# Kernel tuning notes

Hardware: AMD Instinct MI355X
Metric: run time of the kernel (lower is better)

Reference implementation:

```python
import jax, jax.numpy as jnp
import numpy as np

B, NO, NM = 16, 512, 32
DO, DM, DOUT = 128, 64, 128   # in_ope_dim, in_mac_dim, out_mac_dim
H, K = 64, 16                  # external attn: num_heads*coef=8*8, k=dim//num_heads
HID = 128                      # policy hidden dim
NEG = jnp.float32(-1e30)


def _lin(x, W, b=None):
    y = x @ W.T
    return y + b if b is not None else y


def external_attention(x, W_trans, b_trans, W_l0, b_l0, W_l1, b_l1, W_proj, b_proj):
    Bx, N, C = x.shape
    x = _lin(x, W_trans, b_trans)                      # [B,N,8C]
    x = x.reshape(Bx, N, H, K).transpose(0, 2, 1, 3)   # [B,H,N,K]
    attn = _lin(x, W_l0, b_l0)
    attn = jax.nn.softmax(attn, axis=-2)               # softmax over N
    attn = attn / (1e-10 + attn.sum(-1, keepdims=True))
    x = _lin(attn, W_l1, b_l1).transpose(0, 2, 1, 3).reshape(Bx, N, H * K)
    return _lin(x, W_proj, b_proj)                     # [B,N,C]


def gat(adj, feat_ope, feat_mac, Wo, Wm, alpha_o, alpha_m):
    h_ope = feat_ope @ Wo.T                            # [B,No,D]
    h_mac = feat_mac @ Wm.T                            # [B,Nm,D]
    a_o = (h_ope * alpha_o).sum(-1)                    # [B,No]
    a_m = (h_mac * alpha_m).sum(-1)                    # [B,Nm]
    e = adj * (a_o[:, :, None] + a_m[:, None, :])      # [B,No,Nm]
    e = jnp.where(e >= 0, e, 0.2 * e)                  # leaky_relu(0.2)
    mask = adj == 1.0
    e = jnp.where(mask, e, jnp.float32(-9e10))
    alpha = jax.nn.softmax(e, axis=-2) * mask          # softmax over opes
    out_ope = jnp.einsum('bom,bod->bmd', alpha, h_ope) # [B,Nm,D]
    return out_ope + h_mac


def mlp(x, Ws, bs):
    for W, b in zip(Ws[:-1], bs[:-1]):
        x = jnp.tanh(x @ W.T + b)
    return x @ Ws[-1].T + bs[-1]


def setup_inputs() -> dict:
    key = jax.random.key(0)
    ks = jax.random.split(key, 24)
    d = {}
    d['curr_proc_adj'] = jax.random.randint(ks[0], (B, NO, NM), 0, 2).astype(jnp.float32)
    d['norm_opes'] = jax.random.normal(ks[1], (B, NO, DO), jnp.float32)
    d['norm_macs'] = jax.random.normal(ks[2], (B, NM, DM), jnp.float32)
    mask_proc = jax.random.randint(ks[3], (B, NO, NM), 0, 2).astype(bool)
    d['mask_proc'] = mask_proc
    # choose valid (unmasked) actions in the flattened [Nm, No] layout
    mask_flat = jnp.swapaxes(mask_proc, 1, 2).reshape(B, -1)
    d['action_indexes'] = jnp.argmax(mask_flat, axis=1).astype(jnp.int32)
    s = 0.05
    # external attention params (torch Linear: [out,in])
    d['W_trans'] = s * jax.random.normal(ks[4], (DO * 8, DO)); d['b_trans'] = jnp.zeros((DO * 8,))
    d['W_l0'] = s * jax.random.normal(ks[5], (K, K)); d['b_l0'] = jnp.zeros((K,))
    d['W_l1'] = s * jax.random.normal(ks[6], (K, K)); d['b_l1'] = jnp.zeros((K,))
    d['W_proj'] = s * jax.random.normal(ks[7], (DO, DO * 8)); d['b_proj'] = jnp.zeros((DO,))
    # GAT params
    d['Wo'] = s * jax.random.normal(ks[8], (DOUT, DO))
    d['Wm'] = s * jax.random.normal(ks[9], (DOUT, DM))
    d['alpha_o'] = s * jax.random.normal(ks[10], (1, 1, DOUT))
    d['alpha_m'] = s * jax.random.normal(ks[11], (1, 1, DOUT))
    # actor MLP: 512 -> 128 -> 128 -> 1
    d['A0'] = s * jax.random.normal(ks[12], (HID, 2 * DO + 2 * DOUT)); d['Ab0'] = jnp.zeros((HID,))
    d['A1'] = s * jax.random.normal(ks[13], (HID, HID)); d['Ab1'] = jnp.zeros((HID,))
    d['A2'] = s * jax.random.normal(ks[14], (1, HID)); d['Ab2'] = jnp.zeros((1,))
    # critic MLP: 256 -> 128 -> 128 -> 1
    d['C0'] = s * jax.random.normal(ks[15], (HID, DO + DOUT)); d['Cb0'] = jnp.zeros((HID,))
    d['C1'] = s * jax.random.normal(ks[16], (HID, HID)); d['Cb1'] = jnp.zeros((HID,))
    d['C2'] = s * jax.random.normal(ks[17], (1, HID)); d['Cb2'] = jnp.zeros((1,))
    return d


def reference(curr_proc_adj, norm_opes, norm_macs, mask_proc, action_indexes,
              W_trans, b_trans, W_l0, b_l0, W_l1, b_l1, W_proj, b_proj,
              Wo, Wm, alpha_o, alpha_m,
              A0, Ab0, A1, Ab1, A2, Ab2, C0, Cb0, C1, Cb1, C2, Cb2):
    h_opes = external_attention(norm_opes, W_trans, b_trans, W_l0, b_l0,
                                W_l1, b_l1, W_proj, b_proj)      # [B,No,DO]
    h_macs = gat(curr_proc_adj, norm_opes, norm_macs, Wo, Wm, alpha_o, alpha_m)  # [B,Nm,DOUT]
    h_opes_pooled = h_opes.mean(-2)   # [B,DO]
    h_macs_pooled = h_macs.mean(-2)   # [B,DOUT]
    # build h_actions directly in transposed [B, Nm, No, :] layout
    sh_o = (B, NM, NO, DO); sh_m = (B, NM, NO, DOUT)
    h_actions = jnp.concatenate([
        jnp.broadcast_to(h_opes[:, None, :, :], sh_o),
        jnp.broadcast_to(h_macs[:, :, None, :], sh_m),
        jnp.broadcast_to(h_opes_pooled[:, None, None, :], sh_o),
        jnp.broadcast_to(h_macs_pooled[:, None, None, :], sh_m)], axis=-1)
    logits = mlp(h_actions, [A0, A1, A2], [Ab0, Ab1, Ab2]).reshape(B, -1)  # [B, Nm*No]
    mask = jnp.swapaxes(mask_proc, 1, 2).reshape(B, -1)
    logits = jnp.where(mask, logits, NEG)
    logp = jax.nn.log_softmax(logits, axis=1)
    p = jnp.exp(logp)
    action_logprobs = jnp.take_along_axis(logp, action_indexes[:, None], axis=1)[:, 0]
    dist_entropys = -jnp.sum(jnp.where(mask, p * logp, 0.0), axis=1)
    h_pooled = jnp.concatenate([h_opes_pooled, h_macs_pooled], axis=-1)  # [B,256]
    state_values = mlp(h_pooled, [C0, C1, C2], [Cb0, Cb1, Cb2])[:, 0]
    return action_logprobs, state_values, dist_entropys
```

## Files before the change

### kernel.cpp

```cpp
#include <hip/hip_runtime.h>

#define BB 16
#define NO 512
#define NM 32
#define DOC 128
#define C8 1024
#define NH 64
#define KD 16

#define OFF_X12   0
#define OFF_UO    0
#define OFF_LOG   1048576
#define OFF_HOPES 8388608
#define OFF_HOPEG 9437184
#define OFF_HMAC  10485760
#define OFF_HMACS 10551296
#define OFF_AO    10616832
#define OFF_AM    10625024
#define OFF_PO    10625536
#define OFF_PM    10627584
#define OFF_UMHM  10629632
#define OFF_FLAG  10695168
#define OFF_UP    10720000
#define OFF_PART2 10750000
#define OFF_A1P   10900000

using f32x4  = __attribute__((ext_vector_type(4))) float;
using s16x4  = __attribute__((ext_vector_type(4))) short;
using bf16x8 = __attribute__((ext_vector_type(8))) short;

__device__ __forceinline__ float fast_tanh(float x) {
  float e = __expf(2.0f * x);
  return 1.0f - 2.0f * __builtin_amdgcn_rcpf(e + 1.0f);
}

__device__ __forceinline__ short f2bf(float f) {
  unsigned u = __builtin_bit_cast(unsigned, f);
  u += 0x7FFFu + ((u >> 16) & 1u);
  return (short)(u >> 16);
}

__device__ __forceinline__ float bf2f(short s) {
  return __builtin_bit_cast(float, ((unsigned)(unsigned short)s) << 16);
}

__device__ __forceinline__ unsigned cvtpk(float a, float b) {
  unsigned r;
  asm("v_cvt_pk_bf16_f32 %0, %1, %2" : "=v"(r) : "v"(a), "v"(b));
  return r;
}

__device__ __forceinline__ bf16x8 pack8(f32x4 u0, f32x4 u1) {
  union { unsigned u[4]; bf16x8 v; } cv;
  cv.u[0] = cvtpk(u0[0], u0[1]);
  cv.u[1] = cvtpk(u0[2], u0[3]);
  cv.u[2] = cvtpk(u1[0], u1[1]);
  cv.u[3] = cvtpk(u1[2], u1[3]);
  return cv.v;
}

__device__ __forceinline__ bf16x8 pack8f(const float* t) {
  union { unsigned u[4]; bf16x8 v; } cv;
  cv.u[0] = cvtpk(t[0], t[1]);
  cv.u[1] = cvtpk(t[2], t[3]);
  cv.u[2] = cvtpk(t[4], t[5]);
  cv.u[3] = cvtpk(t[6], t[7]);
  return cv.v;
}

__device__ __forceinline__ void smmerge(float& lm, float& lS, float& lT,
                                        float om, float oS, float oT) {
  float nm = fmaxf(lm, om);
  float ea = __expf(lm - nm), eb = __expf(om - nm);
  lT = (lT + (lm - nm) * lS) * ea + (oT + (om - nm) * oS) * eb;
  lS = lS * ea + oS * eb;
  lm = nm;
}

__device__ void probe_body(int tid, const unsigned int* __restrict__ mask,
                           int* __restrict__ flag) {
  __shared__ int s[4];
  int bad = 0;
  for (int i = tid; i < 4096; i += 256) {
    unsigned int v = mask[i];
    if (!(v == 0u || v == 1u || v == 0x3f800000u)) bad = 1;
  }
  unsigned long long any = __ballot(bad);
  int lane = tid & 63, w = tid >> 6;
  if (lane == 0) s[w] = (any != 0ull) ? 1 : 0;
  __syncthreads();
  if (tid == 0) flag[0] = s[0] | s[1] | s[2] | s[3];
}

template<int MT>
__device__ __forceinline__ void loadk(const float* xb, const float* wb,
                                      long sx, long sw, int k0,
                                      f32x4 (&xa)[MT][2], f32x4 (&wa)[4][2]) {
  #pragma unroll
  for (int mi = 0; mi < MT; ++mi) {
    xa[mi][0] = *(const f32x4*)(xb + mi * sx + k0);
    xa[mi][1] = *(const f32x4*)(xb + mi * sx + k0 + 4);
  }
  #pragma unroll
  for (int ni = 0; ni < 4; ++ni) {
    wa[ni][0] = *(const f32x4*)(wb + ni * sw + k0);
    wa[ni][1] = *(const f32x4*)(wb + ni * sw + k0 + 4);
  }
}

template<int MT>
__device__ __forceinline__ void consume(f32x4 (&xa)[MT][2], f32x4 (&wa)[4][2],
                                        f32x4 (&acc)[MT][4]) {
  bf16x8 bfr[4];
  #pragma unroll
  for (int ni = 0; ni < 4; ++ni) bfr[ni] = pack8(wa[ni][0], wa[ni][1]);
  #pragma unroll
  for (int mi = 0; mi < MT; ++mi) {
    bf16x8 af = pack8(xa[mi][0], xa[mi][1]);
    #pragma unroll
    for (int ni = 0; ni < 4; ++ni)
      acc[mi][ni] = __builtin_amdgcn_mfma_f32_16x16x32_bf16(af, bfr[ni], acc[mi][ni], 0, 0, 0);
  }
}

template<int MT>
__device__ void gemm_wave_body(int bx, int by, int tid,
    const float* __restrict__ X, const float* __restrict__ W,
    const float* __restrict__ bias, float* __restrict__ C,
    int N, int Kdim, int ldx, int ldw) {
  const int lane = tid & 63, w = tid >> 6;
  const int rowl = lane & 15, kg = lane >> 4;
  const int n0 = bx * 64;
  const int m0 = (by * 4 + w) * (MT * 16);
  const float* xb = X + (long)(m0 + rowl) * ldx + kg * 8;
  const float* wb = W + (long)(n0 + rowl) * ldw + kg * 8;
  const long sx = (long)16 * ldx, sw = (long)16 * ldw;
  f32x4 acc[MT][4] = {};
  f32x4 A0[MT][2], B0[4][2], A1[MT][2], B1[4][2];
  loadk<MT>(xb, wb, sx, sw, 0, A0, B0);
  for (int k = 0; k < Kdim; k += 64) {
    loadk<MT>(xb, wb, sx, sw, k + 32, A1, B1);
    consume<MT>(A0, B0, acc);
    if (k + 64 < Kdim) loadk<MT>(xb, wb, sx, sw, k + 64, A0, B0);
    consume<MT>(A1, B1, acc);
  }
  #pragma unroll
  for (int mi = 0; mi < MT; ++mi) {
    #pragma unroll
    for (int ni = 0; ni < 4; ++ni) {
      int col = n0 + ni * 16 + rowl;
      float bv = bias ? bias[col] : 0.0f;
      int rb = m0 + mi * 16 + kg * 4;
      #pragma unroll
      for (int r = 0; r < 4; ++r)
        C[(long)(rb + r) * N + col] = acc[mi][ni][r] + bv;
    }
  }
}

template<int MT>
__device__ void gemm_ht_body(int bx, int by, int tid,
    const float* __restrict__ X, const float* __restrict__ W,
    const float* __restrict__ bias, short* __restrict__ Ch,
    int Kdim, int ldx, int ldw) {
  const int lane = tid & 63, w = tid >> 6;
  const int rowl = lane & 15, kg = lane >> 4;
  const int n0 = bx * 64;
  const int m0 = (by * 4 + w) * (MT * 16);
  const float* xb = X + (long)(m0 + rowl) * ldx + kg * 8;
  const float* wb = W + (long)(n0 + rowl) * ldw + kg * 8;
  const long sx = (long)16 * ldx, sw = (long)16 * ldw;
  f32x4 acc[MT][4] = {};
  f32x4 A0[MT][2], B0[4][2], A1[MT][2], B1[4][2];
  loadk<MT>(xb, wb, sx, sw, 0, A0, B0);
  for (int k = 0; k < Kdim; k += 64) {
    loadk<MT>(xb, wb, sx, sw, k + 32, A1, B1);
    consume<MT>(A0, B0, acc);
    if (k + 64 < Kdim) loadk<MT>(xb, wb, sx, sw, k + 64, A0, B0);
    consume<MT>(A1, B1, acc);
  }
  #pragma unroll
  for (int mi = 0; mi < MT; ++mi) {
    #pragma unroll
    for (int ni = 0; ni < 4; ++ni) {
      int col = n0 + ni * 16 + rowl;
      float bv = bias ? bias[col] : 0.0f;
      int h = col >> 4, e = col & 15;
      int rb = m0 + mi * 16 + kg * 4;
      #pragma unroll
      for (int r = 0; r < 4; ++r) {
        int rowI = rb + r;
        int b = rowI >> 9, n = rowI & 511;
        Ch[((long)(b * 64 + h) * 512 + n) * 16 + e] = f2bf(acc[mi][ni][r] + bv);
      }
    }
  }
}

__device__ void convert_a1_body(int blk, int tid,
    const float* __restrict__ A1, short* __restrict__ A1p) {
  int i = blk * 256 + tid;
  int col = i >> 7, k = i & 127;
  A1p[((k >> 3) * 128 + col) * 8 + (k & 7)] = f2bf(A1[i]);
}

__global__ __launch_bounds__(256) void mega1_kernel(
    const float* __restrict__ nop, const float* __restrict__ Wtr,
    const float* __restrict__ btr, short* __restrict__ x12h,
    const float* __restrict__ Wo, float* __restrict__ hopeG,
    const float* __restrict__ nmac, const float* __restrict__ Wm,
    float* __restrict__ hmac,
    const float* __restrict__ A1, short* __restrict__ A1p,
    const unsigned int* __restrict__ mask, int* __restrict__ flag) {
  const int blk = blockIdx.x, tid = threadIdx.x;
  if (blk < 512) {
    gemm_ht_body<4>(blk & 15, blk >> 4, tid, nop, Wtr, btr, x12h, 128, 128, 128);
  } else if (blk < 768) {
    int t = blk - 512;
    gemm_wave_body<1>(t & 1, t >> 1, tid, nop, Wo, nullptr, hopeG, 128, 128, 128, 128);
  } else if (blk < 784) {
    int t = blk - 768;
    gemm_wave_body<1>(t & 1, t >> 1, tid, nmac, Wm, nullptr, hmac, 128, 64, 64, 64);
  } else if (blk < 848) {
    convert_a1_body(blk - 784, tid, A1, A1p);
  } else {
    probe_body(tid, mask, flag);
  }
}

__device__ void attn3_body(int b, int h, int tid, short* __restrict__ x12h,
    const float* __restrict__ W0, const float* __restrict__ b0,
    const float* __restrict__ W1, const float* __restrict__ b1) {
  __shared__ short Pb[4][128 * 16];
  __shared__ float cmw[4][16], csw[4][16];
  const int wq = tid >> 6, lane = tid & 63;
  const int rowl = lane & 15, kg = lane >> 4;
  short* slice = x12h + (long)(b * 64 + h) * 8192;
  const short* wrows = slice + (long)(wq * 128) * 16;
  const bf16x8 zero8 = {};
  bf16x8 xa[8];
  #pragma unroll
  for (int t = 0; t < 8; ++t) {
    if (kg < 2)
      xa[t] = *(const bf16x8*)(wrows + (t * 16 + rowl) * 16 + kg * 8);
    else
      xa[t] = zero8;
  }
  bf16x8 w0f = zero8;
  if (kg < 2) {
    f32x4 a = *(const f32x4*)(W0 + rowl * 16 + kg * 8);
    f32x4 c = *(const f32x4*)(W0 + rowl * 16 + kg * 8 + 4);
    w0f = pack8(a, c);
  }
  const float b0v = b0[rowl];
  f32x4 acc[8];
  #pragma unroll
  for (int t = 0; t < 8; ++t) {
    f32x4 z = {0.f, 0.f, 0.f, 0.f};
    acc[t] = __builtin_amdgcn_mfma_f32_16x16x32_bf16(xa[t], w0f, z, 0, 0, 0);
  }
  float m = -1e30f;
  #pragma unroll
  for (int t = 0; t < 8; ++t)
    #pragma unroll
    for (int r = 0; r < 4; ++r) {
      acc[t][r] += b0v;
      m = fmaxf(m, acc[t][r]);
    }
  m = fmaxf(m, __shfl_xor(m, 16));
  m = fmaxf(m, __shfl_xor(m, 32));
  if (lane < 16) cmw[wq][lane] = m;
  __syncthreads();
  const float cm = fmaxf(fmaxf(cmw[0][rowl], cmw[1][rowl]),
                         fmaxf(cmw[2][rowl], cmw[3][rowl]));
  float s = 0.f;
  #pragma unroll
  for (int t = 0; t < 8; ++t)
    #pragma unroll
    for (int r = 0; r < 4; ++r) {
      float e = __expf(acc[t][r] - cm);
      acc[t][r] = e;
      s += e;
    }
  s += __shfl_xor(s, 16);
  s += __shfl_xor(s, 32);
  if (lane < 16) csw[wq][lane] = s;
  __syncthreads();
  const float cs = csw[0][rowl] + csw[1][rowl] + csw[2][rowl] + csw[3][rowl];
  const float cinv = 1.0f / cs;
  short* pbw = Pb[wq];
  #pragma unroll
  for (int t = 0; t < 8; ++t)
    #pragma unroll
    for (int r = 0; r < 4; ++r) {
      float al = acc[t][r] * cinv;
      float rsv = al;
      rsv += __shfl_xor(rsv, 1);
      rsv += __shfl_xor(rsv, 2);
      rsv += __shfl_xor(rsv, 4);
      rsv += __shfl_xor(rsv, 8);
      float pf = al / (1e-10f + rsv);
      pbw[(t * 16 + kg * 4 + r) * 16 + rowl] = f2bf(pf);
    }
  __syncthreads();
  bf16x8 w1f = zero8;
  if (kg < 2) {
    f32x4 a = *(const f32x4*)(W1 + rowl * 16 + kg * 8);
    f32x4 c = *(const f32x4*)(W1 + rowl * 16 + kg * 8 + 4);
    w1f = pack8(a, c);
  }
  const float b1v = b1[rowl];
  #pragma unroll
  for (int t = 0; t < 8; ++t) {
    bf16x8 pa = zero8;
    if (kg < 2)
      pa = *(const bf16x8*)(pbw + (t * 16 + rowl) * 16 + kg * 8);
    f32x4 z = {0.f, 0.f, 0.f, 0.f};
    f32x4 oacc = __builtin_amdgcn_mfma_f32_16x16x32_bf16(pa, w1f, z, 0, 0, 0);
    #pragma unroll
    for (int r = 0; r < 4; ++r) {
      int n = wq * 128 + t * 16 + kg * 4 + r;
      slice[(long)n * 16 + rowl] = f2bf(oacc[r] + b1v);
    }
  }
}

__global__ __launch_bounds__(256) void mega2_kernel(
    short* __restrict__ x12h,
    const float* __restrict__ W0, const float* __restrict__ b0,
    const float* __restrict__ W1, const float* __restrict__ b1,
    const float* __restrict__ hopeG, const float* __restrict__ alo,
    float* __restrict__ ao,
    const float* __restrict__ hmac, const float* __restrict__ alm,
    float* __restrict__ am) {
  const int blk = blockIdx.x, tid = threadIdx.x;
  if (blk < 1024) {
    attn3_body(blk >> 6, blk & 63, tid, x12h, W0, b0, W1, b1);
  } else {
    int t = blk - 1024;
    int wid = t * 4 + (tid >> 6);
    int lane = tid & 63;
    const float* X; const float* al; float* out; int r;
    if (wid < 8192)       { X = hopeG; al = alo; out = ao; r = wid; }
    else if (wid < 8704)  { X = hmac;  al = alm; out = am; r = wid - 8192; }
    else return;
    const float* row = X + (long)r * 128;
    float v = fmaf(row[lane], al[lane], row[lane + 64] * al[lane + 64]);
    #pragma unroll
    for (int off = 32; off; off >>= 1) v += __shfl_down(v, off);
    if (lane == 0) out[r] = v;
  }
}

__device__ void gemm_hx_body(int bx, int by, int tid,
    const short* __restrict__ Xh, const float* __restrict__ W,
    const float* __restrict__ bias, float* __restrict__ C) {
  const int lane = tid & 63, w = tid >> 6;
  const int rowl = lane & 15, kg = lane >> 4;
  const int n0 = bx * 64;
  const int m0 = (by * 4 + w) * 16;
  const int row = m0 + rowl, b = row >> 9, n = row & 511;
  const short* xb = Xh + (long)b * 524288 + (long)n * 16 + (kg & 1) * 8;
  const long hofs = kg >> 1;
  const float* wb = W + (long)(n0 + rowl) * 1024 + kg * 8;
  const long sw = 16 * 1024L;
  f32x4 acc[4] = {};
  bf16x8 A0, A1;
  f32x4 Wb0[4][2], Wb1[4][2];
  A0 = *(const bf16x8*)(xb + hofs * 8192);
  #pragma unroll
  for (int ni = 0; ni < 4; ++ni) {
    Wb0[ni][0] = *(const f32x4*)(wb + ni * sw);
    Wb0[ni][1] = *(const f32x4*)(wb + ni * sw + 4);
  }
  for (int k = 0; k < 1024; k += 64) {
    A1 = *(const bf16x8*)(xb + (((k + 32) >> 4) + hofs) * 8192);
    #pragma unroll
    for (int ni = 0; ni < 4; ++ni) {
      Wb1[ni][0] = *(const f32x4*)(wb + ni * sw + k + 32);
      Wb1[ni][1] = *(const f32x4*)(wb + ni * sw + k + 36);
    }
    #pragma unroll
    for (int ni = 0; ni < 4; ++ni) {
      bf16x8 bfr = pack8(Wb0[ni][0], Wb0[ni][1]);
      acc[ni] = __builtin_amdgcn_mfma_f32_16x16x32_bf16(A0, bfr, acc[ni], 0, 0, 0);
    }
    if (k + 64 < 1024) {
      A0 = *(const bf16x8*)(xb + (((k + 64) >> 4) + hofs) * 8192);
      #pragma unroll
      for (int ni = 0; ni < 4; ++ni) {
        Wb0[ni][0] = *(const f32x4*)(wb + ni * sw + k + 64);
        Wb0[ni][1] = *(const f32x4*)(wb + ni * sw + k + 68);
      }
    }
    #pragma unroll
    for (int ni = 0; ni < 4; ++ni) {
      bf16x8 bfr = pack8(Wb1[ni][0], Wb1[ni][1]);
      acc[ni] = __builtin_amdgcn_mfma_f32_16x16x32_bf16(A1, bfr, acc[ni], 0, 0, 0);
    }
  }
  #pragma unroll
  for (int ni = 0; ni < 4; ++ni) {
    int col = n0 + ni * 16 + rowl;
    float bv = bias ? bias[col] : 0.0f;
    int rb = m0 + kg * 4;
    #pragma unroll
    for (int r = 0; r < 4; ++r)
      C[(long)(rb + r) * 128 + col] = acc[ni][r] + bv;
  }
}

__device__ void gat_body(int b, int m, int tid,
    const float* __restrict__ adj, const float* __restrict__ ao,
    const float* __restrict__ am, const float* __restrict__ hopeG,
    const float* __restrict__ hmac, float* __restrict__ hmacs) {
  __shared__ float al[NO];
  __shared__ float redA[4], redB[4];
  __shared__ float part[2][128];
  const int lane = tid & 63, w = tid >> 6;
  const float amv = am[b * NM + m];
  float av[2], ev[2];
  float mx = -1e30f;
  #pragma unroll
  for (int i = 0; i < 2; ++i) {
    int o = tid + i * 256;
    float a = adj[(b * NO + o) * NM + m];
    float e = ao[b * NO + o] + amv;
    e = (e >= 0.f) ? e : 0.2f * e;
    av[i] = a; ev[i] = e;
    if (a == 1.0f) mx = fmaxf(mx, e);
  }
  #pragma unroll
  for (int off = 32; off; off >>= 1) mx = fmaxf(mx, __shfl_down(mx, off));
  if (lane == 0) redA[w] = mx;
  __syncthreads();
  mx = fmaxf(fmaxf(redA[0], redA[1]), fmaxf(redA[2], redA[3]));
  float p[2], s = 0.f;
  #pragma unroll
  for (int i = 0; i < 2; ++i) {
    p[i] = (av[i] == 1.0f) ? __expf(ev[i] - mx) : 0.f;
    s += p[i];
  }
  #pragma unroll
  for (int off = 32; off; off >>= 1) s += __shfl_down(s, off);
  if (lane == 0) redB[w] = s;
  __syncthreads();
  s = redB[0] + redB[1] + redB[2] + redB[3];
  const float sinv = (s > 0.f) ? 1.0f / s : 0.f;
  al[tid] = p[0] * sinv;
  al[tid + 256] = p[1] * sinv;
  __syncthreads();
  const int d = tid & 127, og = tid >> 7;
  float acc0 = 0.f, acc1 = 0.f;
  const float* hb = hopeG + ((long)(b * NO) + og * 256) * DOC + d;
  #pragma unroll 8
  for (int i = 0; i < 256; i += 2) {
    acc0 = fmaf(al[og * 256 + i],     hb[(long)i * DOC],       acc0);
    acc1 = fmaf(al[og * 256 + i + 1], hb[(long)(i + 1) * DOC], acc1);
  }
  part[og][d] = acc0 + acc1;
  __syncthreads();
  if (og == 0)
    hmacs[(b * NM + m) * DOC + d] = part[0][d] + part[1][d]
                                   + hmac[(b * NM + m) * DOC + d];
}

__global__ __launch_bounds__(256) void mega3_kernel(
    const short* __restrict__ x12h, const float* __restrict__ Wp,
    const float* __restrict__ bp, float* __restrict__ hopes,
    const float* __restrict__ adj, const float* __restrict__ ao,
    const float* __restrict__ am, const float* __restrict__ hopeG,
    const float* __restrict__ hmac, float* __restrict__ hmacs) {
  const int blk = blockIdx.x, tid = threadIdx.x;
  if (blk < 256) {
    gemm_hx_body(blk & 1, blk >> 1, tid, x12h, Wp, bp, hopes);
  } else {
    int t = blk - 256;
    gat_body(t & 15, t >> 4, tid,
             adj, ao, am, hopeG, hmac, hmacs);
  }
}

__device__ void pool_up_body(int b, int tid,
    const float* __restrict__ hopes, const float* __restrict__ hmacs,
    const float* __restrict__ A0, const float* __restrict__ Ab0,
    float* __restrict__ po, float* __restrict__ pm, float* __restrict__ up) {
  __shared__ float part[2][128];
  __shared__ float pos[128], pms[128];
  const int j = tid & 127, og = tid >> 7;
  const float* hb = hopes + ((long)(b * 512) + og * 256) * 128 + j;
  float a0 = 0.f, a1 = 0.f;
  #pragma unroll 8
  for (int i = 0; i < 256; i += 2) {
    a0 += hb[(long)i * 128];
    a1 += hb[(long)(i + 1) * 128];
  }
  part[og][j] = a0 + a1;
  __syncthreads();
  if (og == 0) {
    float s = (part[0][j] + part[1][j]) * (1.0f / 512.0f);
    po[b * 128 + j] = s;
    pos[j] = s;
  } else {
    const float* mb = hmacs + (long)(b * 32) * 128 + j;
    float t0 = 0.f;
    #pragma unroll 8
    for (int i = 0; i < 32; ++i) t0 += mb[(long)i * 128];
    t0 *= (1.0f / 32.0f);
    pm[b * 128 + j] = t0;
    pms[j] = t0;
  }
  __syncthreads();
  if (tid < 128) {
    const float* a1p = A0 + (long)j * 512 + 256;
    const float* a2p = A0 + (long)j * 512 + 384;
    float acc = Ab0[j];
    #pragma unroll 4
    for (int k4 = 0; k4 < 32; ++k4) {
      f32x4 av = *(const f32x4*)(a1p + k4 * 4);
      acc = fmaf(av[0], pos[k4 * 4], acc);
      acc = fmaf(av[1], pos[k4 * 4 + 1], acc);
      acc = fmaf(av[2], pos[k4 * 4 + 2], acc);
      acc = fmaf(av[3], pos[k4 * 4 + 3], acc);
    }
    #pragma unroll 4
    for (int k4 = 0; k4 < 32; ++k4) {
      f32x4 av = *(const f32x4*)(a2p + k4 * 4);
      acc = fmaf(av[0], pms[k4 * 4], acc);
      acc = fmaf(av[1], pms[k4 * 4 + 1], acc);
      acc = fmaf(av[2], pms[k4 * 4 + 2], acc);
      acc = fmaf(av[3], pms[k4 * 4 + 3], acc);
    }
    up[b * 128 + j] = acc;
  }
}

__global__ __launch_bounds__(256) void mega4_kernel(
    const float* __restrict__ hopes, const float* __restrict__ hmacs,
    const float* __restrict__ A0, const float* __restrict__ Ab0,
    float* __restrict__ po, float* __restrict__ pm, float* __restrict__ up,
    float* __restrict__ Uo, float* __restrict__ umhm) {
  const int blk = blockIdx.x, tid = threadIdx.x;
  if (blk < 16) {
    pool_up_body(blk, tid, hopes, hmacs, A0, Ab0, po, pm, up);
  } else if (blk < 272) {
    int t = blk - 16;
    gemm_wave_body<1>(t & 1, t >> 1, tid, hopes, A0, nullptr, Uo, 128, 128, 128, 512);
  } else {
    int t = blk - 272;
    gemm_wave_body<1>(t & 1, t >> 1, tid, hmacs, A0 + 128, nullptr, umhm, 128, 128, 128, 512);
  }
}

__global__ __launch_bounds__(256) void actor_mfma9_kernel(
    const float* __restrict__ Uo, const float* __restrict__ umhm,
    const float* __restrict__ up, const short* __restrict__ A1p,
    const float* __restrict__ Ab1, const float* __restrict__ A2,
    const float* __restrict__ Ab2, const void* __restrict__ maskp,
    const int* __restrict__ flag, float* __restrict__ logits,
    float* __restrict__ partw) {
  const int tid = threadIdx.x;
  const int blk = blockIdx.x;
  const int oc = blk & 7;
  const int mg = (blk >> 3) & 7;
  const int b  = blk >> 6;
  const int obase = oc * 64;
  const int m0 = mg * 4;
  const int lane = tid & 63, w = tid >> 6;
  const int rowl = lane & 15, kg = lane >> 4;
  const float* uo = Uo + (long)(b * NO + obase + w * 16 + rowl) * 128;
  const float* upb = up + b * 128;
  const float* umb = umhm + (b * NM + m0) * 128;
  bf16x8 af[4][4];
  #pragma unroll
  for (int kk = 0; kk < 4; ++kk) {
    int kb = kk * 32 + kg * 8;
    f32x4 u0 = *(const f32x4*)(uo + kb);
    f32x4 u1 = *(const f32x4*)(uo + kb + 4);
    f32x4 p0 = *(const f32x4*)(upb + kb);
    f32x4 p1 = *(const f32x4*)(upb + kb + 4);
    float base0[4], base1[4];
    #pragma unroll
    for (int e = 0; e < 4; ++e) {
      base0[e] = u0[e] + p0[e];
      base1[e] = u1[e] + p1[e];
    }
    #pragma unroll
    for (int mi = 0; mi < 4; ++mi) {
      f32x4 a0 = *(const f32x4*)(umb + mi * 128 + kb);
      f32x4 a1 = *(const f32x4*)(umb + mi * 128 + kb + 4);
      float t[8];
      #pragma unroll
      for (int e = 0; e < 4; ++e) {
        t[e]     = fast_tanh(base0[e] + a0[e]);
        t[4 + e] = fast_tanh(base1[e] + a1[e]);
      }
      af[mi][kk] = pack8f(t);
    }
  }
  float pr[4][4] = {};
  #pragma unroll
  for (int ct = 0; ct < 8; ++ct) {
    const int col = ct * 16 + rowl;
    bf16x8 bf[4];
    #pragma unroll
    for (int kk = 0; kk < 4; ++kk)
      bf[kk] = *(const bf16x8*)(A1p + ((kk * 4 + kg) * 128 + col) * 8);
    f32x4 ac[4] = {};
    #pragma unroll
    for (int kk = 0; kk < 4; ++kk)
      #pragma unroll
      for (int mi = 0; mi < 4; ++mi)
        ac[mi] = __builtin_amdgcn_mfma_f32_16x16x32_bf16(af[mi][kk], bf[kk], ac[mi], 0, 0, 0);
    const float ab = Ab1[col], a2c = A2[col];
    #pragma unroll
    for (int mi = 0; mi < 4; ++mi)
      #pragma unroll
      for (int r = 0; r < 4; ++r) {
        float z = fast_tanh(ac[mi][r] + ab);
        pr[mi][r] = fmaf(a2c, z, pr[mi][r]);
      }
  }
  const float ab2 = Ab2[0];
  float rv[4][4];
  #pragma unroll
  for (int r = 0; r < 4; ++r) {
    float v0 = pr[0][r], v1 = pr[1][r], v2 = pr[2][r], v3 = pr[3][r];
    #pragma unroll
    for (int off = 1; off < 16; off <<= 1) {
      v0 += __shfl_xor(v0, off);
      v1 += __shfl_xor(v1, off);
      v2 += __shfl_xor(v2, off);
      v3 += __shfl_xor(v3, off);
    }
    rv[r][0] = v0 + ab2; rv[r][1] = v1 + ab2;
    rv[r][2] = v2 + ab2; rv[r][3] = v3 + ab2;
  }
  const long base0 = ((long)b << 14) + (long)m0 * 512 + obase + w * 16 + kg * 4;
  if (rowl == 0) {
    #pragma unroll
    for (int r = 0; r < 4; ++r) {
      logits[base0 + r]        = rv[r][0];
      logits[base0 + 512 + r]  = rv[r][1];
      logits[base0 + 1024 + r] = rv[r][2];
      logits[base0 + 1536 + r] = rv[r][3];
    }
  }
  const bool word_mode = (flag[0] == 0);
  const int ob = obase + w * 16 + kg * 4;
  bool mk[4][4];
  if (word_mode) {
    const unsigned int* mw = (const unsigned int*)maskp;
    #pragma unroll
    for (int r = 0; r < 4; ++r) {
      long mo = (long)(b * NO + ob + r) * NM + m0;
      #pragma unroll
      for (int mi = 0; mi < 4; ++mi) mk[r][mi] = (mw[mo + mi] != 0u);
    }
  } else {
    const unsigned char* mb = (const unsigned char*)maskp;
    #pragma unroll
    for (int r = 0; r < 4; ++r) {
      long mo = (long)(b * NO + ob + r) * NM + m0;
      #pragma unroll
      for (int mi = 0; mi < 4; ++mi) mk[r][mi] = (mb[mo + mi] != 0);
    }
  }
  float lm = -1e30f;
  #pragma unroll
  for (int r = 0; r < 4; ++r)
    #pragma unroll
    for (int mi = 0; mi < 4; ++mi)
      if (mk[r][mi]) lm = fmaxf(lm, rv[r][mi]);
  float lS = 0.f, lT = 0.f;
  #pragma unroll
  for (int r = 0; r < 4; ++r)
    #pragma unroll
    for (int mi = 0; mi < 4; ++mi)
      if (mk[r][mi]) {
        float d = rv[r][mi] - lm;
        float e = __expf(d);
        lS += e; lT += e * d;
      }
  #pragma unroll
  for (int off = 16; off < 64; off <<= 1) {
    float om = __shfl_xor(lm, off);
    float oS = __shfl_xor(lS, off);
    float oT = __shfl_xor(lT, off);
    smmerge(lm, lS, lT, om, oS, oT);
  }
  if (lane == 0) {
    float* pp = partw + ((long)blk * 4 + w) * 3;
    pp[0] = lm; pp[1] = lS; pp[2] = lT;
  }
}

__global__ __launch_bounds__(128) void final2c_kernel(
    const float* __restrict__ part, const float* __restrict__ logits,
    const int* __restrict__ aidx,
    const float* __restrict__ po, const float* __restrict__ pm,
    const float* __restrict__ C0, const float* __restrict__ Cb0,
    const float* __restrict__ C1, const float* __restrict__ Cb1,
    const float* __restrict__ C2, const float* __restrict__ Cb2,
    float* __restrict__ out) {
  if (blockIdx.x < 16) {
    if (threadIdx.x >= 64) return;
    const int b = blockIdx.x;
    const int lane = threadIdx.x;
    float lm = -3e30f, lS = 0.f, lT = 0.f;
    const float* pp = part + ((long)b * 256 + lane * 4) * 3;
    #pragma unroll
    for (int t = 0; t < 4; ++t)
      smmerge(lm, lS, lT, pp[t * 3], pp[t * 3 + 1], pp[t * 3 + 2]);
    #pragma unroll
    for (int off = 1; off < 64; off <<= 1) {
      float om = __shfl_xor(lm, off);
      float oS = __shfl_xor(lS, off);
      float oT = __shfl_xor(lT, off);
      smmerge(lm, lS, lT, om, oS, oT);
    }
    if (lane == 0) {
      float lSm = logf(lS);
      out[b] = logits[b * (NM * NO) + aidx[b]] - lm - lSm;
      out[32 + b] = lSm - lT / lS;
    }
  } else {
    __shared__ float v[256];
    __shared__ float z[128];
    __shared__ float sc[2];
    const int b = blockIdx.x - 16;
    const int j = threadIdx.x;
    v[j] = po[b * 128 + j];
    v[128 + j] = pm[b * 128 + j];
    __syncthreads();
    float acc = Cb0[j];
    for (int k = 0; k < 256; ++k) acc = fmaf(C0[j * 256 + k], v[k], acc);
    z[j] = fast_tanh(acc);
    __syncthreads();
    acc = Cb1[j];
    for (int k = 0; k < 128; ++k) acc = fmaf(C1[j * 128 + k], z[k], acc);
    float z2 = fast_tanh(acc);
    float p = C2[j] * z2;
    #pragma unroll
    for (int off = 32; off; off >>= 1) p += __shfl_down(p, off);
    const int lane = j & 63, w = j >> 6;
    if (lane == 0) sc[w] = p;
    __syncthreads();
    if (j == 0) out[16 + b] = sc[0] + sc[1] + Cb2[0];
  }
}

extern "C" void kernel_launch(void* const* d_in, const int* in_sizes, int n_in,
                              void* d_out, int out_size, void* d_ws, size_t ws_size,
                              hipStream_t stream) {
  (void)in_sizes; (void)n_in; (void)out_size; (void)ws_size;
  const float* adj  = (const float*)d_in[0];
  const float* nop  = (const float*)d_in[1];
  const float* nmac = (const float*)d_in[2];
  const void*  maskp = d_in[3];
  const int*   aidx = (const int*)d_in[4];
  const float* Wtr  = (const float*)d_in[5];
  const float* btr  = (const float*)d_in[6];
  const float* W0   = (const float*)d_in[7];
  const float* b0   = (const float*)d_in[8];
  const float* W1   = (const float*)d_in[9];
  const float* b1   = (const float*)d_in[10];
  const float* Wp   = (const float*)d_in[11];
  const float* bp   = (const float*)d_in[12];
  const float* Wo   = (const float*)d_in[13];
  const float* Wm   = (const float*)d_in[14];
  const float* alo  = (const float*)d_in[15];
  const float* alm  = (const float*)d_in[16];
  const float* A0   = (const float*)d_in[17];
  const float* Ab0  = (const float*)d_in[18];
  const float* A1   = (const float*)d_in[19];
  const float* Ab1  = (const float*)d_in[20];
  const float* A2   = (const float*)d_in[21];
  const float* Ab2  = (const float*)d_in[22];
  const float* C0   = (const float*)d_in[23];
  const float* Cb0  = (const float*)d_in[24];
  const float* C1   = (const float*)d_in[25];
  const float* Cb1  = (const float*)d_in[26];
  const float* C2   = (const float*)d_in[27];
  const float* Cb2  = (const float*)d_in[28];

  float* ws     = (float*)d_ws;
  short* x12h   = (short*)(ws + OFF_X12);
  float* hopes  = ws + OFF_HOPES;
  float* hopeG  = ws + OFF_HOPEG;
  float* hmac   = ws + OFF_HMAC;
  float* hmacs  = ws + OFF_HMACS;
  float* ao     = ws + OFF_AO;
  float* am     = ws + OFF_AM;
  float* po     = ws + OFF_PO;
  float* pm     = ws + OFF_PM;
  float* Uo     = ws + OFF_UO;
  float* umhm   = ws + OFF_UMHM;
  float* logits = ws + OFF_LOG;
  float* up     = ws + OFF_UP;
  short* A1p    = (short*)(ws + OFF_A1P);
  int*   flag   = (int*)(ws + OFF_FLAG);
  float* partw  = ws + OFF_PART2;
  float* outp   = (float*)d_out;

  mega1_kernel<<<849, 256, 0, stream>>>(nop, Wtr, btr, x12h, Wo, hopeG,
                                        nmac, Wm, hmac, A1, A1p,
                                        (const unsigned int*)maskp, flag);
  mega2_kernel<<<3200, 256, 0, stream>>>(x12h, W0, b0, W1, b1,
                                         hopeG, alo, ao, hmac, alm, am);
  mega3_kernel<<<768, 256, 0, stream>>>(x12h, Wp, bp, hopes,
                                        adj, ao, am, hopeG, hmac, hmacs);
  mega4_kernel<<<288, 256, 0, stream>>>(hopes, hmacs, A0, Ab0,
                                        po, pm, up, Uo, umhm);
  actor_mfma9_kernel<<<1024, 256, 0, stream>>>(Uo, umhm, up, A1p, Ab1, A2, Ab2,
                                               maskp, flag, logits, partw);
  final2c_kernel<<<32, 128, 0, stream>>>(partw, logits, aidx,
                                         po, pm, C0, Cb0, C1, Cb1, C2, Cb2, outp);
}
```

Before: 138.7 us.

## Remove final kernel by fusing critic MLP and last-block logsumexp reduction

Moves the critic MLP into the pooling blocks of mega4, which already hold the pooled vectors in shared memory. The per-batch log-softmax combine now runs inside the actor kernel: an atomic counter, zeroed in mega1, lets the last of the 64 blocks per batch merge the partials and write the outputs. This removes one kernel launch and its dependency gap. In exchange it adds threadfence/atomic overhead to every actor block and makes the 16 pooling blocks longer, which may delay mega4 slightly.

```diff
diff --git a/kernel.cpp b/kernel.cpp
--- a/kernel.cpp
+++ b/kernel.cpp
@@ -21,6 +21,7 @@
 #define OFF_PM    10627584
 #define OFF_UMHM  10629632
 #define OFF_FLAG  10695168
+#define OFF_CNT   10695680
 #define OFF_UP    10720000
 #define OFF_PART2 10750000
 #define OFF_A1P   10900000
@@ -78,8 +79,9 @@
 }
 
 __device__ void probe_body(int tid, const unsigned int* __restrict__ mask,
-                           int* __restrict__ flag) {
+                           int* __restrict__ flag, int* __restrict__ cnt) {
   __shared__ int s[4];
+  if (tid < 16) cnt[tid] = 0;
   int bad = 0;
   for (int i = tid; i < 4096; i += 256) {
     unsigned int v = mask[i];
@@ -211,7 +213,8 @@
     const float* __restrict__ nmac, const float* __restrict__ Wm,
     float* __restrict__ hmac,
     const float* __restrict__ A1, short* __restrict__ A1p,
-    const unsigned int* __restrict__ mask, int* __restrict__ flag) {
+    const unsigned int* __restrict__ mask, int* __restrict__ flag,
+    int* __restrict__ cnt) {
   const int blk = blockIdx.x, tid = threadIdx.x;
   if (blk < 512) {
     gemm_ht_body<4>(blk & 15, blk >> 4, tid, nop, Wtr, btr, x12h, 128, 128, 128);
@@ -224,7 +227,7 @@
   } else if (blk < 848) {
     convert_a1_body(blk - 784, tid, A1, A1p);
   } else {
-    probe_body(tid, mask, flag);
+    probe_body(tid, mask, flag, cnt);
   }
 }
 
@@ -484,9 +487,15 @@
 __device__ void pool_up_body(int b, int tid,
     const float* __restrict__ hopes, const float* __restrict__ hmacs,
     const float* __restrict__ A0, const float* __restrict__ Ab0,
-    float* __restrict__ po, float* __restrict__ pm, float* __restrict__ up) {
+    const float* __restrict__ C0, const float* __restrict__ Cb0,
+    const float* __restrict__ C1, const float* __restrict__ Cb1,
+    const float* __restrict__ C2, const float* __restrict__ Cb2,
+    float* __restrict__ po, float* __restrict__ pm, float* __restrict__ up,
+    float* __restrict__ out) {
   __shared__ float part[2][128];
   __shared__ float pos[128], pms[128];
+  __shared__ float zc[128];
+  __shared__ float scc[2];
   const int j = tid & 127, og = tid >> 7;
   const float* hb = hopes + ((long)(b * 512) + og * 256) * 128 + j;
   float a0 = 0.f, a1 = 0.f;
@@ -532,17 +541,39 @@
       acc = fmaf(av[3], pms[k4 * 4 + 3], acc);
     }
     up[b * 128 + j] = acc;
-  }
+    float cacc = Cb0[j];
+    for (int k = 0; k < 128; ++k) cacc = fmaf(C0[j * 256 + k], pos[k], cacc);
+    for (int k = 0; k < 128; ++k) cacc = fmaf(C0[j * 256 + 128 + k], pms[k], cacc);
+    zc[j] = fast_tanh(cacc);
+  }
+  __syncthreads();
+  if (tid < 128) {
+    float acc2 = Cb1[j];
+    for (int k = 0; k < 128; ++k) acc2 = fmaf(C1[j * 128 + k], zc[k], acc2);
+    float z2 = fast_tanh(acc2);
+    float p = C2[j] * z2;
+    #pragma unroll
+    for (int off = 32; off; off >>= 1) p += __shfl_down(p, off);
+    const int lane = tid & 63, w = tid >> 6;
+    if (lane == 0) scc[w] = p;
+  }
+  __syncthreads();
+  if (tid == 0) out[16 + b] = scc[0] + scc[1] + Cb2[0];
 }
 
 __global__ __launch_bounds__(256) void mega4_kernel(
     const float* __restrict__ hopes, const float* __restrict__ hmacs,
     const float* __restrict__ A0, const float* __restrict__ Ab0,
+    const float* __restrict__ C0, const float* __restrict__ Cb0,
+    const float* __restrict__ C1, const float* __restrict__ Cb1,
+    const float* __restrict__ C2, const float* __restrict__ Cb2,
     float* __restrict__ po, float* __restrict__ pm, float* __restrict__ up,
-    float* __restrict__ Uo, float* __restrict__ umhm) {
+    float* __restrict__ Uo, float* __restrict__ umhm,
+    float* __restrict__ out) {
   const int blk = blockIdx.x, tid = threadIdx.x;
   if (blk < 16) {
-    pool_up_body(blk, tid, hopes, hmacs, A0, Ab0, po, pm, up);
+    pool_up_body(blk, tid, hopes, hmacs, A0, Ab0, C0, Cb0, C1, Cb1, C2, Cb2,
+                 po, pm, up, out);
   } else if (blk < 272) {
     int t = blk - 16;
     gemm_wave_body<1>(t & 1, t >> 1, tid, hopes, A0, nullptr, Uo, 128, 128, 128, 512);
@@ -552,13 +583,14 @@
   }
 }
 
-__global__ __launch_bounds__(256) void actor_mfma9_kernel(
+__global__ __launch_bounds__(256) void actor_mfma10_kernel(
     const float* __restrict__ Uo, const float* __restrict__ umhm,
     const float* __restrict__ up, const short* __restrict__ A1p,
     const float* __restrict__ Ab1, const float* __restrict__ A2,
     const float* __restrict__ Ab2, const void* __restrict__ maskp,
-    const int* __restrict__ flag, float* __restrict__ logits,
-    float* __restrict__ partw) {
+    const int* __restrict__ flag, const int* __restrict__ aidx,
+    float* __restrict__ logits, float* __restrict__ partw,
+    int* __restrict__ cnt, float* __restrict__ out) {
   const int tid = threadIdx.x;
   const int blk = blockIdx.x;
   const int oc = blk & 7;
@@ -693,60 +725,33 @@
     float* pp = partw + ((long)blk * 4 + w) * 3;
     pp[0] = lm; pp[1] = lS; pp[2] = lT;
   }
-}
-
-__global__ __launch_bounds__(128) void final2c_kernel(
-    const float* __restrict__ part, const float* __restrict__ logits,
-    const int* __restrict__ aidx,
-    const float* __restrict__ po, const float* __restrict__ pm,
-    const float* __restrict__ C0, const float* __restrict__ Cb0,
-    const float* __restrict__ C1, const float* __restrict__ Cb1,
-    const float* __restrict__ C2, const float* __restrict__ Cb2,
-    float* __restrict__ out) {
-  if (blockIdx.x < 16) {
-    if (threadIdx.x >= 64) return;
-    const int b = blockIdx.x;
-    const int lane = threadIdx.x;
-    float lm = -3e30f, lS = 0.f, lT = 0.f;
-    const float* pp = part + ((long)b * 256 + lane * 4) * 3;
+  __shared__ int sdone;
+  __syncthreads();
+  if (tid == 0) {
+    __threadfence();
+    int old = atomicAdd((int*)&cnt[b], 1);
+    sdone = (old == 63) ? 1 : 0;
+  }
+  __syncthreads();
+  if (sdone && tid < 64) {
+    __threadfence();
+    float fm = -3e30f, fS = 0.f, fT = 0.f;
+    const float* pp = partw + ((long)b * 256 + tid * 4) * 3;
     #pragma unroll
     for (int t = 0; t < 4; ++t)
-      smmerge(lm, lS, lT, pp[t * 3], pp[t * 3 + 1], pp[t * 3 + 2]);
+      smmerge(fm, fS, fT, pp[t * 3], pp[t * 3 + 1], pp[t * 3 + 2]);
     #pragma unroll
     for (int off = 1; off < 64; off <<= 1) {
-      float om = __shfl_xor(lm, off);
-      float oS = __shfl_xor(lS, off);
-      float oT = __shfl_xor(lT, off);
-      smmerge(lm, lS, lT, om, oS, oT);
-    }
-    if (lane == 0) {
-      float lSm = logf(lS);
-      out[b] = logits[b * (NM * NO) + aidx[b]] - lm - lSm;
-      out[32 + b] = lSm - lT / lS;
-    }
-  } else {
-    __shared__ float v[256];
-    __shared__ float z[128];
-    __shared__ float sc[2];
-    const int b = blockIdx.x - 16;
-    const int j = threadIdx.x;
-    v[j] = po[b * 128 + j];
-    v[128 + j] = pm[b * 128 + j];
-    __syncthreads();
-    float acc = Cb0[j];
-    for (int k = 0; k < 256; ++k) acc = fmaf(C0[j * 256 + k], v[k], acc);
-    z[j] = fast_tanh(acc);
-    __syncthreads();
-    acc = Cb1[j];
-    for (int k = 0; k < 128; ++k) acc = fmaf(C1[j * 128 + k], z[k], acc);
-    float z2 = fast_tanh(acc);
-    float p = C2[j] * z2;
-    #pragma unroll
-    for (int off = 32; off; off >>= 1) p += __shfl_down(p, off);
-    const int lane = j & 63, w = j >> 6;
-    if (lane == 0) sc[w] = p;
-    __syncthreads();
-    if (j == 0) out[16 + b] = sc[0] + sc[1] + Cb2[0];
+      float om = __shfl_xor(fm, off);
+      float oS = __shfl_xor(fS, off);
+      float oT = __shfl_xor(fT, off);
+      smmerge(fm, fS, fT, om, oS, oT);
+    }
+    if (tid == 0) {
+      float lSm = logf(fS);
+      out[b] = logits[(long)b * (NM * NO) + aidx[b]] - fm - lSm;
+      out[32 + b] = lSm - fT / fS;
+    }
   }
 }
 
@@ -800,20 +805,21 @@
   float* up     = ws + OFF_UP;
   short* A1p    = (short*)(ws + OFF_A1P);
   int*   flag   = (int*)(ws + OFF_FLAG);
+  int*   cnt    = (int*)(ws + OFF_CNT);
   float* partw  = ws + OFF_PART2;
   float* outp   = (float*)d_out;
 
   mega1_kernel<<<849, 256, 0, stream>>>(nop, Wtr, btr, x12h, Wo, hopeG,
                                         nmac, Wm, hmac, A1, A1p,
-                                        (const unsigned int*)maskp, flag);
+                                        (const unsigned int*)maskp, flag, cnt);
   mega2_kernel<<<3200, 256, 0, stream>>>(x12h, W0, b0, W1, b1,
                                          hopeG, alo, ao, hmac, alm, am);
   mega3_kernel<<<768, 256, 0, stream>>>(x12h, Wp, bp, hopes,
                                         adj, ao, am, hopeG, hmac, hmacs);
   mega4_kernel<<<288, 256, 0, stream>>>(hopes, hmacs, A0, Ab0,
-                                        po, pm, up, Uo, umhm);
-  actor_mfma9_kernel<<<1024, 256, 0, stream>>>(Uo, umhm, up, A1p, Ab1, A2, Ab2,
-                                               maskp, flag, logits, partw);
-  final2c_kernel<<<32, 128, 0, stream>>>(partw, logits, aidx,
-                                         po, pm, C0, Cb0, C1, Cb1, C2, Cb2, outp);
-}
+                                        C0, Cb0, C1, Cb1, C2, Cb2,
+                                        po, pm, up, Uo, umhm, outp);
+  actor_mfma10_kernel<<<1024, 256, 0, stream>>>(Uo, umhm, up, A1p, Ab1, A2, Ab2,
+                                                maskp, flag, aidx,
+                                                logits, partw, cnt, outp);
+}
```

New measurement: 157.3 us. +13.4%, slower.
